# Performance work log

Measured on AMD Instinct MI355X. Metric: run time of the kernel, lower is better.

Reference implementation:

```python
import jax, jax.numpy as jnp
import numpy as np


def _wn(v, g):
    # weight-norm: w[o, i] = g[o] * v[o, i] / ||v[o, :]||
    return g[:, None] * v / jnp.linalg.norm(v, axis=1, keepdims=True)


def setup_inputs() -> dict:
    key = jax.random.key(0)
    ks = jax.random.split(key, 8)
    B, C, H, W = 16, 512, 64, 64
    K, D = 2048, 64
    return {
        "z": jax.random.normal(ks[0], (B, C, H, W), dtype=jnp.float32),
        "codebook": jax.random.normal(ks[1], (K, D), dtype=jnp.float32),
        "in_v": jax.random.normal(ks[2], (D, C), dtype=jnp.float32),
        "in_g": jax.random.uniform(ks[3], (D,), dtype=jnp.float32, minval=0.5, maxval=1.5),
        "in_b": jax.random.normal(ks[4], (D,), dtype=jnp.float32) * 0.02,
        "out_v": jax.random.normal(ks[5], (C, D), dtype=jnp.float32),
        "out_g": jax.random.uniform(ks[6], (C,), dtype=jnp.float32, minval=0.5, maxval=1.5),
        "out_b": jax.random.normal(ks[7], (C,), dtype=jnp.float32) * 0.02,
    }


def reference(z, codebook, in_v, in_g, in_b, out_v, out_g, out_b):
    COMMIT_W = 0.25
    B, C, H, W = z.shape
    D = codebook.shape[1]

    Wi = _wn(in_v, in_g)    # [D, C]
    Wo = _wn(out_v, out_g)  # [C, D]

    # in_proj (1x1 conv): b c h w -> b d h w
    z_e = jnp.einsum('bchw,dc->bdhw', z, Wi) + in_b[None, :, None, None]

    # flatten tokens: (b h w) d
    z_e_flat = z_e.transpose(0, 2, 3, 1).reshape(-1, D)

    dist = (jnp.sum(z_e_flat * z_e_flat, axis=1, keepdims=True)
            - 2.0 * z_e_flat @ codebook.T
            + jnp.sum(codebook * codebook, axis=1)[None, :])
    indices_flat = jnp.argmin(dist, axis=1)            # [(BHW)]
    indices = indices_flat.reshape(B, H, W)

    z_q_flat = codebook[indices_flat]                  # gather [(BHW), D]
    z_q = z_q_flat.reshape(B, H, W, D).transpose(0, 3, 1, 2)  # b d h w

    sg = jax.lax.stop_gradient
    commitment_loss = jnp.mean((sg(z_e) - z_q) ** 2)
    codebook_loss = jnp.mean((sg(z_q) - z_e) ** 2)
    vq_loss = codebook_loss + COMMIT_W * commitment_loss

    # straight-through
    z_q_st = z_e + sg(z_q - z_e)

    # out_proj (1x1 conv): b d h w -> b c h w
    out = jnp.einsum('bdhw,cd->bchw', z_q_st, Wo) + out_b[None, :, None, None]
    return out, indices, vq_loss
```

## Files before the change

### kernel.cpp

```cpp
#include <hip/hip_runtime.h>
#include <math.h>


typedef __attribute__((address_space(1))) const unsigned int* gas_ptr;
typedef __attribute__((address_space(3))) unsigned int* las_ptr;
#define GLD_LDS16(gsrc, ldst) \
  __builtin_amdgcn_global_load_lds((gas_ptr)(const void*)(gsrc), \
                                   (las_ptr)(void*)(ldst), 16, 0, 0)


__global__ void k_prep_wi(const float* __restrict__ v, const float* __restrict__ g,
                          float* __restrict__ wiT){
  const int d = blockIdx.x;
  const int tid = threadIdx.x;
  float s = 0.f;
  for (int c = tid; c < 512; c += 256){ float x = v[d*512+c]; s = fmaf(x,x,s); }
  __shared__ float red[4];
  #pragma unroll
  for (int o = 32; o > 0; o >>= 1) s += __shfl_down(s, o);
  if ((tid & 63) == 0) red[tid >> 6] = s;
  __syncthreads();
  const float nrm = sqrtf(red[0]+red[1]+red[2]+red[3]);
  const float gd = g[d];
  for (int c = tid; c < 512; c += 256) wiT[c*64 + d] = gd * v[d*512+c] / nrm;
}

__global__ void k_prep_wo(const float* __restrict__ v, const float* __restrict__ g,
                          float* __restrict__ wot){
  const int c = blockIdx.x;
  const int d = threadIdx.x;
  const float x = v[c*64+d];
  float s = x*x;
  #pragma unroll
  for (int o = 32; o > 0; o >>= 1) s += __shfl_down(s, o);
  const float nrm = __shfl(sqrtf(s), 0);
  wot[d*512 + c] = g[c] * x / nrm;
}

__global__ void k_table(const float* __restrict__ cbk, const float* __restrict__ wot,
                        const float* __restrict__ ob, float* __restrict__ table,
                        float* __restrict__ ne, float* __restrict__ cbm2T){
  const int k = blockIdx.x;
  const int tid = threadIdx.x;
  __shared__ float e[64];
  if (tid < 64) e[tid] = cbk[k*64 + tid];
  __syncthreads();
  if (tid < 64){
    float x = e[tid];
    cbm2T[tid*2048 + k] = -2.0f * x;
    float s = x*x;
    #pragma unroll
    for (int o = 32; o > 0; o >>= 1) s += __shfl_down(s, o);
    if (tid == 0) ne[k] = s;
  }
  const int c = tid;
  float acc = ob[c];
  #pragma unroll 16
  for (int d = 0; d < 64; d++) acc = fmaf(e[d], wot[d*512 + c], acc);
  table[(size_t)k*512 + c] = acc;
}

__global__ __launch_bounds__(256, 2) void k_main(
    const float* __restrict__ z, const float* __restrict__ wiT,
    const float* __restrict__ inb, const float* __restrict__ cbm2T,
    const float* __restrict__ cbk, const float* __restrict__ ne,
    const float* __restrict__ table, float* __restrict__ out,
    float* __restrict__ oidx, double* __restrict__ loss)
{
  __shared__ __align__(16) float ze_s[64*68];
  __shared__ __align__(16) float rgb[2*2176];
  __shared__ int bidx_s[64];

  const int tid  = threadIdx.x;
  const int w    = tid >> 6;
  const int lane = tid & 63;
  const int t0   = blockIdx.x << 6;
  const int b    = t0 >> 12;
  const int hw0  = t0 & 4095;
  const float* zb = z + ((size_t)b << 21) + hw0;

  const int tg  = tid & 15;
  const int dgp = tid >> 4;

  const int srow = w*4 + (lane >> 4);
  const int scol = (lane & 15) << 2;

  float acc1[4][4];
  #pragma unroll
  for (int i = 0; i < 4; i++)
    #pragma unroll
    for (int j = 0; j < 4; j++) acc1[i][j] = 0.f;

  GLD_LDS16(zb + (size_t)srow*4096 + scol,  &rgb[0*2176 + w*256]);
  GLD_LDS16(wiT + srow*64 + scol,           &rgb[0*2176 + 1024 + w*256]);
  __syncthreads();

  for (int c = 0; c < 32; c++){
    const int buf = c & 1;
    if (c < 31){
      const int c0n = (c+1) << 4;
      GLD_LDS16(zb + (size_t)(c0n + srow)*4096 + scol, &rgb[(buf^1)*2176 + w*256]);
      GLD_LDS16(wiT + (c0n + srow)*64 + scol,          &rgb[(buf^1)*2176 + 1024 + w*256]);
    }
    const float* zc = &rgb[buf*2176];
    const float* wc = &rgb[buf*2176 + 1024];
    #pragma unroll 4
    for (int cc = 0; cc < 16; cc++){
      const float4 ta = *(const float4*)&zc[cc*64 + tg*4];
      const float4 wv = *(const float4*)&wc[cc*64 + dgp*4];
      acc1[0][0]=fmaf(ta.x,wv.x,acc1[0][0]); acc1[0][1]=fmaf(ta.y,wv.x,acc1[0][1]);
      acc1[0][2]=fmaf(ta.z,wv.x,acc1[0][2]); acc1[0][3]=fmaf(ta.w,wv.x,acc1[0][3]);
      acc1[1][0]=fmaf(ta.x,wv.y,acc1[1][0]); acc1[1][1]=fmaf(ta.y,wv.y,acc1[1][1]);
      acc1[1][2]=fmaf(ta.z,wv.y,acc1[1][2]); acc1[1][3]=fmaf(ta.w,wv.y,acc1[1][3]);
      acc1[2][0]=fmaf(ta.x,wv.z,acc1[2][0]); acc1[2][1]=fmaf(ta.y,wv.z,acc1[2][1]);
      acc1[2][2]=fmaf(ta.z,wv.z,acc1[2][2]); acc1[2][3]=fmaf(ta.w,wv.z,acc1[2][3]);
      acc1[3][0]=fmaf(ta.x,wv.w,acc1[3][0]); acc1[3][1]=fmaf(ta.y,wv.w,acc1[3][1]);
      acc1[3][2]=fmaf(ta.z,wv.w,acc1[3][2]); acc1[3][3]=fmaf(ta.w,wv.w,acc1[3][3]);
    }
    __syncthreads();
  }

  #pragma unroll
  for (int i = 0; i < 4; i++){
    const int d = dgp*4 + i;
    const float bd = inb[d];
    float4 o = {acc1[i][0]+bd, acc1[i][1]+bd, acc1[i][2]+bd, acc1[i][3]+bd};
    *(float4*)&ze_s[d*68 + tg*4] = o;
  }
  __syncthreads();

  const int kg = dgp;
  float best[4]; int bidx[4];
  #pragma unroll
  for (int j = 0; j < 4; j++){ best[j] = INFINITY; bidx[j] = 0; }

  {
    const float* gbs = cbm2T + (size_t)(2*w)*2048 + lane*4;
    GLD_LDS16(gbs,        &rgb[0*2176 + (2*w)  *272]);
    GLD_LDS16(gbs + 2048, &rgb[0*2176 + (2*w+1)*272]);
  }
  __syncthreads();

#define P2(CV, I) \
  acc[0][I]=fmaf(za.x,CV,acc[0][I]); acc[1][I]=fmaf(za.y,CV,acc[1][I]); \
  acc[2][I]=fmaf(za.z,CV,acc[2][I]); acc[3][I]=fmaf(za.w,CV,acc[3][I]);

  float acc[4][16];
  for (int s = 0; s < 64; s++){
    const int buf = s & 1;
    const int dq = s & 7, kc = (s >> 3) << 8;
    if (s < 63){
      const int s1 = s + 1;
      const int ndq = s1 & 7, nkc = (s1 >> 3) << 8;
      const float* gbs = cbm2T + (size_t)(ndq*8 + 2*w)*2048 + nkc + lane*4;
      GLD_LDS16(gbs,        &rgb[(buf^1)*2176 + (2*w)  *272]);
      GLD_LDS16(gbs + 2048, &rgb[(buf^1)*2176 + (2*w+1)*272]);
    }
    if (dq == 0){
      #pragma unroll
      for (int q = 0; q < 4; q++){
        const float4 nv = *(const float4*)&ne[kc + kg*16 + q*4];
        acc[0][q*4  ]=nv.x; acc[1][q*4  ]=nv.x; acc[2][q*4  ]=nv.x; acc[3][q*4  ]=nv.x;
        acc[0][q*4+1]=nv.y; acc[1][q*4+1]=nv.y; acc[2][q*4+1]=nv.y; acc[3][q*4+1]=nv.y;
        acc[0][q*4+2]=nv.z; acc[1][q*4+2]=nv.z; acc[2][q*4+2]=nv.z; acc[3][q*4+2]=nv.z;
        acc[0][q*4+3]=nv.w; acc[1][q*4+3]=nv.w; acc[2][q*4+3]=nv.w; acc[3][q*4+3]=nv.w;
      }
    }
    const float* cbf = &rgb[buf*2176];
    const int dbase = dq << 3;
    #pragma unroll
    for (int d = 0; d < 8; d++){
      const int dr = dbase + d;
      const float4 za = *(const float4*)&ze_s[dr*68 + tg*4];
      const float4 c0 = *(const float4*)&cbf[d*272 + kg*16];
      const float4 c1 = *(const float4*)&cbf[d*272 + kg*16 + 4];
      const float4 c2 = *(const float4*)&cbf[d*272 + kg*16 + 8];
      const float4 c3 = *(const float4*)&cbf[d*272 + kg*16 + 12];
      P2(c0.x, 0)  P2(c0.y, 1)  P2(c0.z, 2)  P2(c0.w, 3)
      P2(c1.x, 4)  P2(c1.y, 5)  P2(c1.z, 6)  P2(c1.w, 7)
      P2(c2.x, 8)  P2(c2.y, 9)  P2(c2.z,10)  P2(c2.w,11)
      P2(c3.x,12)  P2(c3.y,13)  P2(c3.z,14)  P2(c3.w,15)
    }
    if (dq == 7){
      #pragma unroll
      for (int i = 0; i < 16; i++){
        const int k = kc + kg*16 + i;
        #pragma unroll
        for (int j = 0; j < 4; j++)
          if (acc[j][i] < best[j]){ best[j] = acc[j][i]; bidx[j] = k; }
      }
    }
    __syncthreads();
  }
#undef P2

  float* rb = rgb;
  int*   ri = (int*)(rgb + 1024);
  #pragma unroll
  for (int j = 0; j < 4; j++){
    const int t = tg*4 + j;
    rb[t*16 + kg] = best[j];
    ri[t*16 + kg] = bidx[j];
  }
  __syncthreads();

  if (tid < 64){
    const int t = tid;
    float bv = rb[t*16]; int bi = ri[t*16];
    #pragma unroll
    for (int q = 1; q < 16; q++){
      const float vq = rb[t*16 + q]; const int iq = ri[t*16 + q];
      if (vq < bv || (vq == bv && iq < bi)){ bv = vq; bi = iq; }
    }
    bidx_s[t] = bi;
    oidx[t0 + t] = (float)bi;
    float myloss = 0.f;
    const float* e = cbk + (size_t)bi * 64;
    #pragma unroll 8
    for (int d = 0; d < 64; d++){
      const float diff = ze_s[d*68 + t] - e[d];
      myloss = fmaf(diff, diff, myloss);
    }
    #pragma unroll
    for (int o = 32; o > 0; o >>= 1) myloss += __shfl_down(myloss, o);
    if (t == 0) atomicAdd(loss, (double)myloss);
  }
  __syncthreads();

  {
    const int tl = tid & 63, cg = tid >> 6;
    const int myk = bidx_s[tl];
    const float* trow = table + ((size_t)myk << 9) + cg*128;
    float* ob = out + (((size_t)b) << 21) + hw0 + tl;
    #pragma unroll 4
    for (int ci = 0; ci < 32; ci++){
      const float4 v = *(const float4*)(trow + ci*4);
      const size_t cbase = (size_t)(cg*128 + ci*4) << 12;
      ob[cbase        ] = v.x;
      ob[cbase +  4096] = v.y;
      ob[cbase +  8192] = v.z;
      ob[cbase + 12288] = v.w;
    }
  }
}

__global__ void k_finish(const double* __restrict__ loss, float* __restrict__ oloss){
  *oloss = (float)(1.25 * (*loss) / 4194304.0);
}


extern "C" void kernel_launch(void* const* d_in, const int* in_sizes, int n_in,
                              void* d_out, int out_size, void* d_ws, size_t ws_size,
                              hipStream_t stream) {
  const float* z   = (const float*)d_in[0];
  const float* cbk = (const float*)d_in[1];
  const float* inv = (const float*)d_in[2];
  const float* ing = (const float*)d_in[3];
  const float* inb = (const float*)d_in[4];
  const float* ov  = (const float*)d_in[5];
  const float* og  = (const float*)d_in[6];
  const float* ob  = (const float*)d_in[7];

  float* ws    = (float*)d_ws;
  float* wiT   = ws;
  float* wot   = ws + 32768;
  float* table = ws + 65536;
  float* ne    = ws + 65536 + 1048576;
  double* loss = (double*)(ws + 1116160);
  float* cbm2T = ws + 1179648;

  float* out   = (float*)d_out;
  float* oidx  = out + 33554432;
  float* oloss = out + 33619968;

  hipMemsetAsync(loss, 0, sizeof(double), stream);
  k_prep_wi<<<64, 256, 0, stream>>>(inv, ing, wiT);
  k_prep_wo<<<512, 64, 0, stream>>>(ov, og, wot);
  k_table<<<2048, 512, 0, stream>>>(cbk, wot, ob, table, ne, cbm2T);
  k_main<<<1024, 256, 0, stream>>>(z, wiT, inb, cbm2T, cbk, ne, table, out, oidx, loss);
  k_finish<<<1, 1, 0, stream>>>(loss, oloss);
}
```

Baseline: 326.0 us.

## Hold token features in registers and scan codebook split across waves

The distance/argmin stage is restructured. Each thread now keeps its token's 64-dim projected feature in registers. Each wave scans a quarter of the codebook, reading row-major codebook rows with wave-uniform (scalar/broadcast) loads instead of staging a transposed codebook through LDS with double buffering. This removes the per-step LDS traffic and barriers, and the codebook is now stored row-major. The cost is 64 extra VGPRs per thread, a longer serial dependency chain per distance, and a tie-breaking rule that no longer compares indices across waves.

```diff
diff --git a/kernel.cpp b/kernel.cpp
--- a/kernel.cpp
+++ b/kernel.cpp
@@ -39,7 +39,7 @@
 
 __global__ void k_table(const float* __restrict__ cbk, const float* __restrict__ wot,
                         const float* __restrict__ ob, float* __restrict__ table,
-                        float* __restrict__ ne, float* __restrict__ cbm2T){
+                        float* __restrict__ ne, float* __restrict__ cbm2){
   const int k = blockIdx.x;
   const int tid = threadIdx.x;
   __shared__ float e[64];
@@ -47,7 +47,7 @@
   __syncthreads();
   if (tid < 64){
     float x = e[tid];
-    cbm2T[tid*2048 + k] = -2.0f * x;
+    cbm2[(size_t)k*64 + tid] = -2.0f * x;
     float s = x*x;
     #pragma unroll
     for (int o = 32; o > 0; o >>= 1) s += __shfl_down(s, o);
@@ -62,7 +62,7 @@
 
 __global__ __launch_bounds__(256, 2) void k_main(
     const float* __restrict__ z, const float* __restrict__ wiT,
-    const float* __restrict__ inb, const float* __restrict__ cbm2T,
+    const float* __restrict__ inb, const float* __restrict__ cbm2,
     const float* __restrict__ cbk, const float* __restrict__ ne,
     const float* __restrict__ table, float* __restrict__ out,
     float* __restrict__ oidx, double* __restrict__ loss)
@@ -129,96 +129,60 @@
   }
   __syncthreads();
 
-  const int kg = dgp;
-  float best[4]; int bidx[4];
-  #pragma unroll
-  for (int j = 0; j < 4; j++){ best[j] = INFINITY; bidx[j] = 0; }
-
-  {
-    const float* gbs = cbm2T + (size_t)(2*w)*2048 + lane*4;
-    GLD_LDS16(gbs,        &rgb[0*2176 + (2*w)  *272]);
-    GLD_LDS16(gbs + 2048, &rgb[0*2176 + (2*w+1)*272]);
-  }
-  __syncthreads();
-
-#define P2(CV, I) \
-  acc[0][I]=fmaf(za.x,CV,acc[0][I]); acc[1][I]=fmaf(za.y,CV,acc[1][I]); \
-  acc[2][I]=fmaf(za.z,CV,acc[2][I]); acc[3][I]=fmaf(za.w,CV,acc[3][I]);
-
-  float acc[4][16];
-  for (int s = 0; s < 64; s++){
-    const int buf = s & 1;
-    const int dq = s & 7, kc = (s >> 3) << 8;
-    if (s < 63){
-      const int s1 = s + 1;
-      const int ndq = s1 & 7, nkc = (s1 >> 3) << 8;
-      const float* gbs = cbm2T + (size_t)(ndq*8 + 2*w)*2048 + nkc + lane*4;
-      GLD_LDS16(gbs,        &rgb[(buf^1)*2176 + (2*w)  *272]);
-      GLD_LDS16(gbs + 2048, &rgb[(buf^1)*2176 + (2*w+1)*272]);
-    }
-    if (dq == 0){
-      #pragma unroll
-      for (int q = 0; q < 4; q++){
-        const float4 nv = *(const float4*)&ne[kc + kg*16 + q*4];
-        acc[0][q*4  ]=nv.x; acc[1][q*4  ]=nv.x; acc[2][q*4  ]=nv.x; acc[3][q*4  ]=nv.x;
-        acc[0][q*4+1]=nv.y; acc[1][q*4+1]=nv.y; acc[2][q*4+1]=nv.y; acc[3][q*4+1]=nv.y;
-        acc[0][q*4+2]=nv.z; acc[1][q*4+2]=nv.z; acc[2][q*4+2]=nv.z; acc[3][q*4+2]=nv.z;
-        acc[0][q*4+3]=nv.w; acc[1][q*4+3]=nv.w; acc[2][q*4+3]=nv.w; acc[3][q*4+3]=nv.w;
-      }
-    }
-    const float* cbf = &rgb[buf*2176];
-    const int dbase = dq << 3;
-    #pragma unroll
-    for (int d = 0; d < 8; d++){
-      const int dr = dbase + d;
-      const float4 za = *(const float4*)&ze_s[dr*68 + tg*4];
-      const float4 c0 = *(const float4*)&cbf[d*272 + kg*16];
-      const float4 c1 = *(const float4*)&cbf[d*272 + kg*16 + 4];
-      const float4 c2 = *(const float4*)&cbf[d*272 + kg*16 + 8];
-      const float4 c3 = *(const float4*)&cbf[d*272 + kg*16 + 12];
-      P2(c0.x, 0)  P2(c0.y, 1)  P2(c0.z, 2)  P2(c0.w, 3)
-      P2(c1.x, 4)  P2(c1.y, 5)  P2(c1.z, 6)  P2(c1.w, 7)
-      P2(c2.x, 8)  P2(c2.y, 9)  P2(c2.z,10)  P2(c2.w,11)
-      P2(c3.x,12)  P2(c3.y,13)  P2(c3.z,14)  P2(c3.w,15)
-    }
-    if (dq == 7){
-      #pragma unroll
-      for (int i = 0; i < 16; i++){
-        const int k = kc + kg*16 + i;
-        #pragma unroll
-        for (int j = 0; j < 4; j++)
-          if (acc[j][i] < best[j]){ best[j] = acc[j][i]; bidx[j] = k; }
-      }
-    }
-    __syncthreads();
-  }
-#undef P2
+  const int q = __builtin_amdgcn_readfirstlane(tid >> 6);
+  const int t = tid & 63;
+
+  float ze_r[64];
+  #pragma unroll
+  for (int d = 0; d < 64; d++) ze_r[d] = ze_s[d*68 + t];
+
+  float best = INFINITY; int bi = 0;
+  const float* __restrict__ cq  = cbm2 + ((size_t)q << 9) * 64;
+  const float* __restrict__ neq = ne + (q << 9);
+
+  for (int kk = 0; kk < 512; kk += 2){
+    const float2 nv = *(const float2*)&neq[kk];
+    const float* r0 = cq + (size_t)kk * 64;
+    float d0 = nv.x, d1 = nv.y;
+    #pragma unroll
+    for (int j = 0; j < 16; j++){
+      const float4 a = *(const float4*)(r0 + 4*j);
+      const float4 bq = *(const float4*)(r0 + 64 + 4*j);
+      const int db = 4*j;
+      d0 = fmaf(ze_r[db  ], a.x, d0);
+      d0 = fmaf(ze_r[db+1], a.y, d0);
+      d0 = fmaf(ze_r[db+2], a.z, d0);
+      d0 = fmaf(ze_r[db+3], a.w, d0);
+      d1 = fmaf(ze_r[db  ], bq.x, d1);
+      d1 = fmaf(ze_r[db+1], bq.y, d1);
+      d1 = fmaf(ze_r[db+2], bq.z, d1);
+      d1 = fmaf(ze_r[db+3], bq.w, d1);
+    }
+    const int k = (q << 9) + kk;
+    if (d0 < best){ best = d0; bi = k; }
+    if (d1 < best){ best = d1; bi = k + 1; }
+  }
 
   float* rb = rgb;
-  int*   ri = (int*)(rgb + 1024);
-  #pragma unroll
-  for (int j = 0; j < 4; j++){
-    const int t = tg*4 + j;
-    rb[t*16 + kg] = best[j];
-    ri[t*16 + kg] = bidx[j];
-  }
+  int*   ri = (int*)(rgb + 256);
+  rb[q*64 + t] = best;
+  ri[q*64 + t] = bi;
   __syncthreads();
 
   if (tid < 64){
-    const int t = tid;
-    float bv = rb[t*16]; int bi = ri[t*16];
-    #pragma unroll
-    for (int q = 1; q < 16; q++){
-      const float vq = rb[t*16 + q]; const int iq = ri[t*16 + q];
-      if (vq < bv || (vq == bv && iq < bi)){ bv = vq; bi = iq; }
-    }
-    bidx_s[t] = bi;
-    oidx[t0 + t] = (float)bi;
+    float bv = rb[t]; int bfin = ri[t];
+    #pragma unroll
+    for (int qq = 1; qq < 4; qq++){
+      const float vq = rb[qq*64 + t]; const int iq = ri[qq*64 + t];
+      if (vq < bv){ bv = vq; bfin = iq; }
+    }
+    bidx_s[t] = bfin;
+    oidx[t0 + t] = (float)bfin;
     float myloss = 0.f;
-    const float* e = cbk + (size_t)bi * 64;
+    const float* e = cbk + (size_t)bfin * 64;
     #pragma unroll 8
     for (int d = 0; d < 64; d++){
-      const float diff = ze_s[d*68 + t] - e[d];
+      const float diff = ze_r[d] - e[d];
       myloss = fmaf(diff, diff, myloss);
     }
     #pragma unroll
@@ -267,7 +231,7 @@
   float* table = ws + 65536;
   float* ne    = ws + 65536 + 1048576;
   double* loss = (double*)(ws + 1116160);
-  float* cbm2T = ws + 1179648;
+  float* cbm2  = ws + 1179648;
 
   float* out   = (float*)d_out;
   float* oidx  = out + 33554432;
@@ -276,7 +240,7 @@
   hipMemsetAsync(loss, 0, sizeof(double), stream);
   k_prep_wi<<<64, 256, 0, stream>>>(inv, ing, wiT);
   k_prep_wo<<<512, 64, 0, stream>>>(ov, og, wot);
-  k_table<<<2048, 512, 0, stream>>>(cbk, wot, ob, table, ne, cbm2T);
-  k_main<<<1024, 256, 0, stream>>>(z, wiT, inb, cbm2T, cbk, ne, table, out, oidx, loss);
+  k_table<<<2048, 512, 0, stream>>>(cbk, wot, ob, table, ne, cbm2);
+  k_main<<<1024, 256, 0, stream>>>(z, wiT, inb, cbm2, cbk, ne, table, out, oidx, loss);
   k_finish<<<1, 1, 0, stream>>>(loss, oloss);
 }
```

Measured after the change: 466.6 us. +43.1%, slower.
